# Kernel optimization log

Hardware: AMD Instinct MI355X
Metric: run time of the kernel (lower is better)

## Reference

```python
import jax, jax.numpy as jnp
import numpy as np

B, N, D, H = 2, 2048, 1024, 16
DH = D // H  # 64


def setup_inputs() -> dict:
    key = jax.random.key(0)
    k1, k2, k3, k4, k5 = jax.random.split(key, 5)
    x = jax.random.normal(k1, (B, N, D), dtype=jnp.float32)
    # per-head kqv Linear weights, stacked: [H, D, 3*DH] (acts as x @ W)
    W_kqv = jax.random.normal(k2, (H, D, 3 * DH), dtype=jnp.float32) * 0.02
    b_kqv = jax.random.normal(k3, (H, 3 * DH), dtype=jnp.float32) * 0.02
    W_proj = jax.random.normal(k4, (D, D), dtype=jnp.float32) * 0.02
    b_proj = jax.random.normal(k5, (D,), dtype=jnp.float32) * 0.02
    return {"x": x, "W_kqv": W_kqv, "b_kqv": b_kqv, "W_proj": W_proj, "b_proj": b_proj}


def reference(x, W_kqv, b_kqv, W_proj, b_proj):
    # per-head projections, all heads batched: [B, H, N, 3*DH]
    kqv = jnp.einsum('bnd,hde->bhne', x, W_kqv) + b_kqv[None, :, None, :]
    # original chunk order is k, q, v
    k, q, v = jnp.split(kqv, 3, axis=-1)  # each [B, H, N, DH]
    # scores: A = q @ k^T / sqrt(DH)  -> [B, H, N, N]
    A = jnp.einsum('bhnd,bhmd->bhnm', q, k) / jnp.sqrt(jnp.asarray(DH, x.dtype))
    causal = jnp.tril(jnp.ones((N, N), dtype=bool))
    A = jnp.where(causal[None, None, :, :], A, -jnp.inf)
    attn = jax.nn.softmax(A, axis=-1)
    sa = jnp.einsum('bhnm,bhmd->bhnd', attn, v)          # [B, H, N, DH]
    sa = sa.transpose(0, 2, 1, 3).reshape(B, N, D)        # concat heads
    out = sa @ W_proj.T + b_proj                          # output projection
    return out
```

## Files before the change

kernel.cpp:

```cpp
#include <hip/hip_runtime.h>
#include <hip/hip_bf16.h>
#include <cstdint>
#include <cstddef>

#define B_  2
#define N_  2048
#define D_  1024
#define H_  16
#define DH_ 64
#define E3_ 192

typedef __attribute__((ext_vector_type(8))) short short8;
typedef __attribute__((ext_vector_type(8))) unsigned short ushort8v;
typedef __attribute__((ext_vector_type(4))) float floatx4;

static __device__ __forceinline__ unsigned short f2bf(float f) {
  union { float f; unsigned u; } c; c.f = f;
  unsigned r = c.u + 0x7fffu + ((c.u >> 16) & 1u);
  return (unsigned short)(r >> 16);
}

#define MFMA(a,b,c) __builtin_amdgcn_mfma_f32_16x16x32_bf16((a),(b),(c),0,0,0)

#define GL_LDS16(g, l) __builtin_amdgcn_global_load_lds( \
    (const __attribute__((address_space(1))) void*)(g),  \
    (__attribute__((address_space(3))) void*)(l), 16, 0, 0)

__global__ __launch_bounds__(256) void k_prep(const float* __restrict__ x,
                                              const float* __restrict__ Wkqv,
                                              const float* __restrict__ Wproj,
                                              unsigned short* __restrict__ Xb,
                                              unsigned short* __restrict__ Wt,
                                              unsigned short* __restrict__ Wpb) {
  __shared__ float tile[64][65];
  int bx = blockIdx.x, t = threadIdx.x;
  if (bx < 2048 || bx >= 2816) {
    const float* in = (bx < 2048) ? x : Wproj;
    unsigned short* out = (bx < 2048) ? Xb : Wpb;
    int i = ((bx < 2048) ? bx : bx - 2816) * 256 + t;
    const float4* p = (const float4*)in + (size_t)i * 2;
    float4 a = p[0], b = p[1];
    ushort8v o;
    o[0]=f2bf(a.x); o[1]=f2bf(a.y); o[2]=f2bf(a.z); o[3]=f2bf(a.w);
    o[4]=f2bf(b.x); o[5]=f2bf(b.y); o[6]=f2bf(b.z); o[7]=f2bf(b.w);
    *((ushort8v*)out + i) = o;
    return;
  }
  int idx = bx - 2048;
  int d0 = (idx & 15) * 64, rem = idx >> 4;
  int cat = rem % 3, h = rem / 3, e0 = cat * 64;
  const float* Wp = Wkqv + (size_t)h * D_ * E3_;
  int dr = t >> 2, ec = (t & 3) * 16;
#pragma unroll
  for (int j = 0; j < 16; j += 4) {
    float4 wv = *(const float4*)&Wp[(size_t)(d0 + dr) * E3_ + e0 + ec + j];
    tile[dr][ec + j + 0] = wv.x; tile[dr][ec + j + 1] = wv.y;
    tile[dr][ec + j + 2] = wv.z; tile[dr][ec + j + 3] = wv.w;
  }
  __syncthreads();
  int er = t >> 2, dc = (t & 3) * 16;
  ushort8v o0, o1;
#pragma unroll
  for (int j = 0; j < 8; j++) o0[j] = f2bf(tile[dc + j][er]);
#pragma unroll
  for (int j = 0; j < 8; j++) o1[j] = f2bf(tile[dc + 8 + j][er]);
  size_t o = ((size_t)(cat * 1024 + h * 64 + er)) * D_ + d0 + dc;
  *(ushort8v*)&Wt[o]     = o0;
  *(ushort8v*)&Wt[o + 8] = o1;
}

__global__ __launch_bounds__(512, 2) void k_qkv(const unsigned short* __restrict__ Xb,
                                                const unsigned short* __restrict__ Wt,
                                                const float* __restrict__ bkqv,
                                                unsigned short* __restrict__ Qb,
                                                unsigned short* __restrict__ Kb,
                                                unsigned short* __restrict__ Vt) {
  __shared__ unsigned short LDSf[65536];
  const int t = threadIdx.x;
  const int wid = t >> 6, lane = t & 63, quad = lane >> 4, l16 = lane & 15;
  const int wr = wid >> 2, wc = wid & 3;
  const int m0 = blockIdx.x * 256, c0 = blockIdx.y * 256;

  floatx4 acc[8][4];
#pragma unroll
  for (int i = 0; i < 8; i++)
#pragma unroll
    for (int j = 0; j < 4; j++) acc[i][j] = (floatx4){0.f, 0.f, 0.f, 0.f};

  const int slr = t >> 3;
  const int sco = ((t & 7) ^ (slr & 7)) * 8;
  const unsigned short* gA0 = Xb + (size_t)(m0 +   0 + slr) * D_ + sco;
  const unsigned short* gA1 = Xb + (size_t)(m0 +  64 + slr) * D_ + sco;
  const unsigned short* gA2 = Xb + (size_t)(m0 + 128 + slr) * D_ + sco;
  const unsigned short* gA3 = Xb + (size_t)(m0 + 192 + slr) * D_ + sco;
  const unsigned short* gB0 = Wt + (size_t)(c0 +   0 + slr) * D_ + sco;
  const unsigned short* gB1 = Wt + (size_t)(c0 +  64 + slr) * D_ + sco;
  const unsigned short* gB2 = Wt + (size_t)(c0 + 128 + slr) * D_ + sco;
  const unsigned short* gB3 = Wt + (size_t)(c0 + 192 + slr) * D_ + sco;
#define SA(gp, q, s, bb) GL_LDS16((gp) + (s) * 64, &LDSf[(bb) * 16384 + (q) * 4096 + t * 8])
#define SB(gp, q, s, bb) GL_LDS16((gp) + (s) * 64, &LDSf[32768 + (bb) * 16384 + (q) * 4096 + t * 8])

  const int aoff0 = ((quad)     ^ (l16 & 7)) * 8;
  const int aoff1 = ((4 + quad) ^ (l16 & 7)) * 8;
  const unsigned short* Abase = &LDSf[(wr * 128 + l16) * 64];
  const unsigned short* Bbase = &LDSf[32768 + (wc * 64 + l16) * 64];

  SA(gA0, 0, 0, 0); SA(gA1, 1, 0, 0); SA(gA2, 2, 0, 0); SA(gA3, 3, 0, 0);
  SB(gB0, 0, 0, 0); SB(gB1, 1, 0, 0); SB(gB2, 2, 0, 0); SB(gB3, 3, 0, 0);
  SA(gA0, 0, 1, 1); SA(gA2, 2, 1, 1);
  asm volatile("s_waitcnt vmcnt(2)" ::: "memory");
  __builtin_amdgcn_s_barrier();

  for (int s = 0; s < 16; s++) {
    const int buf = s & 1, nbuf = buf ^ 1;
    const int so = buf * 16384;
    short8 a[4][2], b[4][2];
#pragma unroll
    for (int mi = 0; mi < 4; mi++) {
      a[mi][0] = *(const short8*)&Abase[so + mi * 1024 + aoff0];
      a[mi][1] = *(const short8*)&Abase[so + mi * 1024 + aoff1];
    }
#pragma unroll
    for (int ni = 0; ni < 2; ni++) {
      b[ni][0] = *(const short8*)&Bbase[so + ni * 1024 + aoff0];
      b[ni][1] = *(const short8*)&Bbase[so + ni * 1024 + aoff1];
    }
    if (s < 15) {
      SA(gA1, 1, s + 1, nbuf); SA(gA3, 3, s + 1, nbuf);
      SB(gB0, 0, s + 1, nbuf); SB(gB1, 1, s + 1, nbuf);
      SB(gB2, 2, s + 1, nbuf); SB(gB3, 3, s + 1, nbuf);
    }
    __builtin_amdgcn_s_barrier();
    asm volatile("s_waitcnt lgkmcnt(0)" ::: "memory");
    __builtin_amdgcn_sched_barrier(0);
    __builtin_amdgcn_s_setprio(1);
#pragma unroll
    for (int mi = 0; mi < 4; mi++)
#pragma unroll
      for (int ni = 0; ni < 2; ni++) {
        acc[mi][ni] = MFMA(a[mi][0], b[ni][0], acc[mi][ni]);
        acc[mi][ni] = MFMA(a[mi][1], b[ni][1], acc[mi][ni]);
      }
    __builtin_amdgcn_s_setprio(0);
    __builtin_amdgcn_s_barrier();
#pragma unroll
    for (int ni = 2; ni < 4; ni++) {
      b[ni][0] = *(const short8*)&Bbase[so + ni * 1024 + aoff0];
      b[ni][1] = *(const short8*)&Bbase[so + ni * 1024 + aoff1];
    }
    __builtin_amdgcn_s_barrier();
    asm volatile("s_waitcnt lgkmcnt(0)" ::: "memory");
    __builtin_amdgcn_sched_barrier(0);
    __builtin_amdgcn_s_setprio(1);
#pragma unroll
    for (int mi = 0; mi < 4; mi++)
#pragma unroll
      for (int ni = 2; ni < 4; ni++) {
        acc[mi][ni] = MFMA(a[mi][0], b[ni][0], acc[mi][ni]);
        acc[mi][ni] = MFMA(a[mi][1], b[ni][1], acc[mi][ni]);
      }
    __builtin_amdgcn_s_setprio(0);
    __builtin_amdgcn_s_barrier();
#pragma unroll
    for (int mi = 0; mi < 4; mi++) {
      a[mi][0] = *(const short8*)&Abase[so + (mi + 4) * 1024 + aoff0];
      a[mi][1] = *(const short8*)&Abase[so + (mi + 4) * 1024 + aoff1];
    }
    if (s < 14) { SA(gA0, 0, s + 2, buf); SA(gA2, 2, s + 2, buf); }
    __builtin_amdgcn_s_barrier();
    asm volatile("s_waitcnt lgkmcnt(0)" ::: "memory");
    __builtin_amdgcn_sched_barrier(0);
    __builtin_amdgcn_s_setprio(1);
#pragma unroll
    for (int mi = 0; mi < 4; mi++)
#pragma unroll
      for (int ni = 0; ni < 2; ni++) {
        acc[mi + 4][ni] = MFMA(a[mi][0], b[ni][0], acc[mi + 4][ni]);
        acc[mi + 4][ni] = MFMA(a[mi][1], b[ni][1], acc[mi + 4][ni]);
      }
    __builtin_amdgcn_s_setprio(0);
    __builtin_amdgcn_s_barrier();
    __builtin_amdgcn_s_setprio(1);
#pragma unroll
    for (int mi = 0; mi < 4; mi++)
#pragma unroll
      for (int ni = 2; ni < 4; ni++) {
        acc[mi + 4][ni] = MFMA(a[mi][0], b[ni][0], acc[mi + 4][ni]);
        acc[mi + 4][ni] = MFMA(a[mi][1], b[ni][1], acc[mi + 4][ni]);
      }
    __builtin_amdgcn_s_setprio(0);
    if (s < 14) { asm volatile("s_waitcnt vmcnt(2)" ::: "memory"); }
    else        { asm volatile("s_waitcnt vmcnt(0)" ::: "memory"); }
    __builtin_amdgcn_s_barrier();
  }

  __syncthreads();
  unsigned short* scr = &LDSf[wid * 8192];
  const int cat = c0 >> 10;
  const int h   = ((c0 + wc * 64) >> 6) & 15;
  const int bb  = (m0 + wr * 128) >> 11;
  const int n0b = (m0 + wr * 128) & (N_ - 1);
  const int l8 = lane & 7, lh = lane >> 3;
  if (cat < 2) {
    const float scale = (cat == 1) ? 0.18033688011112042f : 1.0f;
    float bias[4];
#pragma unroll
    for (int ni = 0; ni < 4; ni++) bias[ni] = bkqv[h * E3_ + cat * 64 + ni * 16 + l16];
#pragma unroll
    for (int mi = 0; mi < 8; mi++)
#pragma unroll
      for (int ni = 0; ni < 4; ni++)
#pragma unroll
        for (int r = 0; r < 4; r++) {
          int rl = mi * 16 + quad * 4 + r, cl = ni * 16 + l16;
          scr[rl * 64 + ((((cl >> 3) ^ rl) & 7) * 8) + (cl & 7)] =
              f2bf((acc[mi][ni][r] + bias[ni]) * scale);
        }
    asm volatile("s_waitcnt lgkmcnt(0)" ::: "memory");
    unsigned short* dst = (cat == 0) ? Kb : Qb;
#pragma unroll
    for (int j = 0; j < 16; j++) {
      int rl = j * 8 + lh;
      short8 vv = *(const short8*)&scr[rl * 64 + ((l8 ^ lh) * 8)];
      *(short8*)&dst[((size_t)(bb * H_ + h) * N_ + n0b + rl) * DH_ + l8 * 8] = vv;
    }
  } else {
    float bias[4];
#pragma unroll
    for (int ni = 0; ni < 4; ni++) bias[ni] = bkqv[h * E3_ + 128 + ni * 16 + l16];
#pragma unroll
    for (int mi = 0; mi < 8; mi++)
#pragma unroll
      for (int ni = 0; ni < 4; ni++)
#pragma unroll
        for (int r = 0; r < 4; r++) {
          int nl = mi * 16 + quad * 4 + r, e = ni * 16 + l16;
          scr[e * 128 + ((((nl >> 3) ^ e) & 15) * 8) + (nl & 7)] =
              f2bf(acc[mi][ni][r] + bias[ni]);
        }
    asm volatile("s_waitcnt lgkmcnt(0)" ::: "memory");
#pragma unroll
    for (int j = 0; j < 16; j++) {
      int e = (j & 7) * 8 + lh;
      int nc = l8 + (j >> 3) * 8;
      short8 vv = *(const short8*)&scr[e * 128 + (((nc ^ e) & 15) * 8)];
      *(short8*)&Vt[((size_t)(bb * H_ + h) * DH_ + e) * N_ + n0b + nc * 8] = vv;
    }
  }
#undef SA
#undef SB
}

__global__ __launch_bounds__(256) void k_flash(const unsigned short* __restrict__ Qb,
                                               const unsigned short* __restrict__ Kb,
                                               const unsigned short* __restrict__ Vt,
                                               unsigned short* __restrict__ sab) {
  int bh = blockIdx.x;
  int yr = blockIdx.y, g = yr >> 3, o = yr & 7;
  int qb = (g == 0) ? o : (g == 1) ? 31 - o : (g == 2) ? 8 + o : 23 - o;
  int q0b = qb * 64;
  int wave = threadIdx.x >> 6;
  int lane = threadIdx.x & 63, quad = lane >> 4, l16 = lane & 15;
  const unsigned short* Qp = Qb + (size_t)bh * N_ * DH_;
  const unsigned short* Kp = Kb + (size_t)bh * N_ * DH_;
  const unsigned short* Vp = Vt + (size_t)bh * DH_ * N_;
  __shared__ unsigned short Klds[2][2 * 64 * 32];
  __shared__ unsigned short Vlds[2][2 * 64 * 32];
  __shared__ unsigned short Plds[4][16 * 64];
  unsigned short* P = Plds[wave];

  int q0w = q0b + wave * 16;
  short8 qf0 = *(const short8*)&Qp[(q0w + l16) * DH_ + quad * 8];
  short8 qf1 = *(const short8*)&Qp[(q0w + l16) * DH_ + 32 + quad * 8];

  int swz = ((lane & 3) ^ ((lane >> 3) & 3)) * 8;
  const unsigned short* gK = Kp + (size_t)(wave * 16 + (lane >> 2)) * DH_ + swz;
  const unsigned short* gV = Vp + (size_t)(wave * 16 + (lane >> 2)) * N_ + swz;
  int lofs = (wave * 16) * 32;
  int xr = ((l16 >> 1) & 3) * 8;
  int pxr = l16 & 7;

#define FSTAGE(ii, bb) do {                                              \
    size_t ko_ = (size_t)(ii) * 64 * DH_; int vo_ = (ii) * 64;           \
    GL_LDS16(gK + ko_,      &Klds[bb][lofs]);                            \
    GL_LDS16(gK + ko_ + 32, &Klds[bb][lofs + 64 * 32]);                  \
    GL_LDS16(gV + vo_,      &Vlds[bb][lofs]);                            \
    GL_LDS16(gV + vo_ + 32, &Vlds[bb][lofs + 64 * 32]);                  \
  } while (0)

  floatx4 O[4];
  float lr[4];
#pragma unroll
  for (int r = 0; r < 4; r++) { O[r] = (floatx4){0.f, 0.f, 0.f, 0.f}; lr[r] = 0.f; }

  int nt = (q0b >> 6) + 1;
  FSTAGE(0, 0);
  if (nt > 1) FSTAGE(1, 1);

  for (int i = 0; i < nt; i++) {
    int buf = i & 1;
    if (i + 1 < nt) { asm volatile("s_waitcnt vmcnt(4)" ::: "memory"); }
    else            { asm volatile("s_waitcnt vmcnt(0)" ::: "memory"); }
    __builtin_amdgcn_s_barrier();
    __builtin_amdgcn_sched_barrier(0);
    short8 kf[4][2], vf[4][2];
#pragma unroll
    for (int c = 0; c < 4; c++) {
      kf[c][0] = *(const short8*)&Klds[buf][(c * 16 + l16) * 32 + ((quad * 8) ^ xr)];
      kf[c][1] = *(const short8*)&Klds[buf][(64 + c * 16 + l16) * 32 + ((quad * 8) ^ xr)];
      vf[c][0] = *(const short8*)&Vlds[buf][(c * 16 + l16) * 32 + ((quad * 8) ^ xr)];
      vf[c][1] = *(const short8*)&Vlds[buf][(64 + c * 16 + l16) * 32 + ((quad * 8) ^ xr)];
    }
    floatx4 s[4];
#pragma unroll
    for (int c = 0; c < 4; c++) {
      s[c] = (floatx4){0.f, 0.f, 0.f, 0.f};
      s[c] = MFMA(qf0, kf[c][0], s[c]);
      s[c] = MFMA(qf1, kf[c][1], s[c]);
    }
    if (i == nt - 1) {
#pragma unroll
      for (int c = 0; c < 4; c++)
#pragma unroll
        for (int r = 0; r < 4; r++) {
          int row = wave * 16 + quad * 4 + r;
          if (c * 16 + l16 > row) s[c][r] = -1e30f;
        }
    }
#pragma unroll
    for (int c = 0; c < 4; c++)
#pragma unroll
      for (int r = 0; r < 4; r++)
        s[c][r] = __builtin_amdgcn_exp2f(s[c][r]);
#pragma unroll
    for (int r = 0; r < 4; r++)
      lr[r] += (s[0][r] + s[1][r]) + (s[2][r] + s[3][r]);
#pragma unroll
    for (int c = 0; c < 4; c++) {
      int ch = c * 2 + (l16 >> 3);
#pragma unroll
      for (int r = 0; r < 4; r++) {
        int row = quad * 4 + r;
        P[row * 64 + ((ch ^ (row & 7)) * 8) + (l16 & 7)] = f2bf(s[c][r]);
      }
    }
    __asm__ volatile("s_waitcnt lgkmcnt(0)" ::: "memory");
    short8 pa0 = *(const short8*)&P[l16 * 64 + ((quad ^ pxr) * 8)];
    short8 pa1 = *(const short8*)&P[l16 * 64 + (((quad + 4) ^ pxr) * 8)];
    __asm__ volatile("" ::: "memory");
#pragma unroll
    for (int dt = 0; dt < 4; dt++) {
      O[dt] = MFMA(pa0, vf[dt][0], O[dt]);
      O[dt] = MFMA(pa1, vf[dt][1], O[dt]);
    }
    __builtin_amdgcn_s_barrier();
    __builtin_amdgcn_sched_barrier(0);
    if (i + 2 < nt) FSTAGE(i + 2, buf);
  }
#undef FSTAGE

#pragma unroll
  for (int m = 1; m < 16; m <<= 1)
#pragma unroll
    for (int r = 0; r < 4; r++) lr[r] += __shfl_xor(lr[r], m);

  int b = bh >> 4, h = bh & 15;
#pragma unroll
  for (int r = 0; r < 4; r++) {
    float inv = 1.0f / lr[r];
    size_t base = ((size_t)b * N_ + q0w + quad * 4 + r) * D_ + h * DH_;
#pragma unroll
    for (int dt = 0; dt < 4; dt++) sab[base + dt * 16 + l16] = f2bf(O[dt][r] * inv);
  }
}

__global__ __launch_bounds__(256) void k_proj(const unsigned short* __restrict__ sab,
                                              const unsigned short* __restrict__ Wpb,
                                              const float* __restrict__ bproj,
                                              float* __restrict__ out) {
  __shared__ unsigned short Alds[2][2][64 * 32];
  __shared__ unsigned short Blds[2][2][64 * 32];
  int t = threadIdx.x;
  int m0 = blockIdx.x * 64, c0 = blockIdx.y * 64;
  int wave = t >> 6, lane = t & 63, quad = lane >> 4, l16 = lane & 15;
  int wm = (wave >> 1) * 32, wn = (wave & 1) * 32;
  floatx4 acc[2][2];
#pragma unroll
  for (int i = 0; i < 2; i++) { acc[i][0] = (floatx4){0,0,0,0}; acc[i][1] = (floatx4){0,0,0,0}; }

  int swz = ((lane & 3) ^ ((lane >> 3) & 3)) * 8;
  const unsigned short* gA = sab + (size_t)(m0 + wave * 16 + (lane >> 2)) * D_ + swz;
  const unsigned short* gB = Wpb + (size_t)(c0 + wave * 16 + (lane >> 2)) * D_ + swz;
  int lofs = (wave * 16) * 32;
  int xr = ((l16 >> 1) & 3) * 8;

  GL_LDS16(gA,      &Alds[0][0][lofs]);
  GL_LDS16(gA + 32, &Alds[0][1][lofs]);
  GL_LDS16(gB,      &Blds[0][0][lofs]);
  GL_LDS16(gB + 32, &Blds[0][1][lofs]);

  for (int i = 0; i < 16; i++) {
    int buf = i & 1;
    __syncthreads();
    if (i + 1 < 16) {
      int k0 = (i + 1) * 64;
      GL_LDS16(gA + k0,      &Alds[buf ^ 1][0][lofs]);
      GL_LDS16(gA + k0 + 32, &Alds[buf ^ 1][1][lofs]);
      GL_LDS16(gB + k0,      &Blds[buf ^ 1][0][lofs]);
      GL_LDS16(gB + k0 + 32, &Blds[buf ^ 1][1][lofs]);
    }
#pragma unroll
    for (int kk = 0; kk < 2; kk++) {
      short8 a[2], b[2];
#pragma unroll
      for (int mi = 0; mi < 2; mi++) a[mi] = *(const short8*)&Alds[buf][kk][(wm + mi * 16 + l16) * 32 + ((quad * 8) ^ xr)];
#pragma unroll
      for (int ni = 0; ni < 2; ni++) b[ni] = *(const short8*)&Blds[buf][kk][(wn + ni * 16 + l16) * 32 + ((quad * 8) ^ xr)];
#pragma unroll
      for (int mi = 0; mi < 2; mi++)
#pragma unroll
        for (int ni = 0; ni < 2; ni++) acc[mi][ni] = MFMA(a[mi], b[ni], acc[mi][ni]);
    }
  }
#pragma unroll
  for (int mi = 0; mi < 2; mi++)
#pragma unroll
    for (int ni = 0; ni < 2; ni++) {
      int col = c0 + wn + ni * 16 + l16;
      int grow = m0 + wm + mi * 16 + quad * 4;
      float bias = bproj[col];
#pragma unroll
      for (int r = 0; r < 4; r++)
        out[(size_t)(grow + r) * D_ + col] = acc[mi][ni][r] + bias;
    }
}

extern "C" void kernel_launch(void* const* d_in, const int* in_sizes, int n_in,
                              void* d_out, int out_size, void* d_ws, size_t ws_size,
                              hipStream_t stream) {
  const float* x     = (const float*)d_in[0];
  const float* Wkqv  = (const float*)d_in[1];
  const float* bkqv  = (const float*)d_in[2];
  const float* Wproj = (const float*)d_in[3];
  const float* bproj = (const float*)d_in[4];
  float* out = (float*)d_out;

  char* w = (char*)d_ws;
  unsigned short* Xb  = (unsigned short*)(w);
  unsigned short* Wt  = (unsigned short*)(w + (8u  << 20));
  unsigned short* Wpb = (unsigned short*)(w + (14u << 20));
  unsigned short* Qb  = (unsigned short*)(w + (16u << 20));
  unsigned short* Kb  = (unsigned short*)(w + (24u << 20));
  unsigned short* Vt  = (unsigned short*)(w + (32u << 20));
  unsigned short* sa  = (unsigned short*)(w + (40u << 20));

  k_prep<<<2048 + 768 + 512, 256, 0, stream>>>(x, Wkqv, Wproj, Xb, Wt, Wpb);
  k_qkv<<<dim3(B_ * N_ / 256, 3072 / 256), 512, 0, stream>>>(Xb, Wt, bkqv, Qb, Kb, Vt);
  k_flash<<<dim3(B_ * H_, N_ / 64), 256, 0, stream>>>(Qb, Kb, Vt, sa);
  k_proj<<<dim3(B_ * N_ / 64, D_ / 64), 256, 0, stream>>>(sa, Wpb, bproj, out);
}
```

Before: 172.5 us.

## Retile output projection GEMM to 128x128 blocks with deeper prefetch; add MFMA setprio

The output projection kernel moves from 64x64 tiles with 4 waves to 128x128 tiles with 8 waves. It uses a single swizzled LDS buffer with a two-stage-ahead global_load_lds prefetch and explicit vmcnt waits, which raises operand reuse per load and reduces global traffic. The flash-attention and projection MFMA sections are also wrapped in s_setprio raises so waves doing matrix math are favored. The trade-offs are fewer blocks (256 instead of 1024), which may leave CUs underused, and higher register and LDS pressure per block.

```diff
diff --git a/kernel.cpp b/kernel.cpp
--- a/kernel.cpp
+++ b/kernel.cpp
@@ -312,12 +312,14 @@
       vf[c][1] = *(const short8*)&Vlds[buf][(64 + c * 16 + l16) * 32 + ((quad * 8) ^ xr)];
     }
     floatx4 s[4];
+    __builtin_amdgcn_s_setprio(1);
 #pragma unroll
     for (int c = 0; c < 4; c++) {
       s[c] = (floatx4){0.f, 0.f, 0.f, 0.f};
       s[c] = MFMA(qf0, kf[c][0], s[c]);
       s[c] = MFMA(qf1, kf[c][1], s[c]);
     }
+    __builtin_amdgcn_s_setprio(0);
     if (i == nt - 1) {
 #pragma unroll
       for (int c = 0; c < 4; c++)
@@ -348,11 +350,13 @@
     short8 pa0 = *(const short8*)&P[l16 * 64 + ((quad ^ pxr) * 8)];
     short8 pa1 = *(const short8*)&P[l16 * 64 + (((quad + 4) ^ pxr) * 8)];
     __asm__ volatile("" ::: "memory");
+    __builtin_amdgcn_s_setprio(1);
 #pragma unroll
     for (int dt = 0; dt < 4; dt++) {
       O[dt] = MFMA(pa0, vf[dt][0], O[dt]);
       O[dt] = MFMA(pa1, vf[dt][1], O[dt]);
     }
+    __builtin_amdgcn_s_setprio(0);
     __builtin_amdgcn_s_barrier();
     __builtin_amdgcn_sched_barrier(0);
     if (i + 2 < nt) FSTAGE(i + 2, buf);
@@ -374,65 +378,88 @@
   }
 }
 
-__global__ __launch_bounds__(256) void k_proj(const unsigned short* __restrict__ sab,
+__global__ __launch_bounds__(512) void k_proj(const unsigned short* __restrict__ sab,
                                               const unsigned short* __restrict__ Wpb,
                                               const float* __restrict__ bproj,
                                               float* __restrict__ out) {
-  __shared__ unsigned short Alds[2][2][64 * 32];
-  __shared__ unsigned short Blds[2][2][64 * 32];
-  int t = threadIdx.x;
-  int m0 = blockIdx.x * 64, c0 = blockIdx.y * 64;
-  int wave = t >> 6, lane = t & 63, quad = lane >> 4, l16 = lane & 15;
-  int wm = (wave >> 1) * 32, wn = (wave & 1) * 32;
-  floatx4 acc[2][2];
-#pragma unroll
-  for (int i = 0; i < 2; i++) { acc[i][0] = (floatx4){0,0,0,0}; acc[i][1] = (floatx4){0,0,0,0}; }
-
-  int swz = ((lane & 3) ^ ((lane >> 3) & 3)) * 8;
-  const unsigned short* gA = sab + (size_t)(m0 + wave * 16 + (lane >> 2)) * D_ + swz;
-  const unsigned short* gB = Wpb + (size_t)(c0 + wave * 16 + (lane >> 2)) * D_ + swz;
-  int lofs = (wave * 16) * 32;
-  int xr = ((l16 >> 1) & 3) * 8;
-
-  GL_LDS16(gA,      &Alds[0][0][lofs]);
-  GL_LDS16(gA + 32, &Alds[0][1][lofs]);
-  GL_LDS16(gB,      &Blds[0][0][lofs]);
-  GL_LDS16(gB + 32, &Blds[0][1][lofs]);
+  __shared__ unsigned short LDSp[32768];
+  const int t = threadIdx.x;
+  const int wid = t >> 6, lane = t & 63, quad = lane >> 4, l16 = lane & 15;
+  const int wr = wid >> 1, wc = wid & 1;
+  const int bid = blockIdx.x;
+  const int m0 = (bid >> 3) * 128, c0 = (bid & 7) * 128;
+
+  floatx4 acc[2][4];
+#pragma unroll
+  for (int i = 0; i < 2; i++)
+#pragma unroll
+    for (int j = 0; j < 4; j++) acc[i][j] = (floatx4){0.f, 0.f, 0.f, 0.f};
+
+  const int slr = t >> 3;
+  const int sco = ((t & 7) ^ (slr & 7)) * 8;
+  const unsigned short* gA0 = sab + (size_t)(m0 +  0 + slr) * D_ + sco;
+  const unsigned short* gA1 = sab + (size_t)(m0 + 64 + slr) * D_ + sco;
+  const unsigned short* gB0 = Wpb + (size_t)(c0 +  0 + slr) * D_ + sco;
+  const unsigned short* gB1 = Wpb + (size_t)(c0 + 64 + slr) * D_ + sco;
+#define PA(gp, q, s, bb) GL_LDS16((gp) + (s) * 64, &LDSp[(bb) * 8192 + (q) * 4096 + t * 8])
+#define PB(gp, q, s, bb) GL_LDS16((gp) + (s) * 64, &LDSp[16384 + (bb) * 8192 + (q) * 4096 + t * 8])
+
+  const int aoff0 = ((quad)     ^ (l16 & 7)) * 8;
+  const int aoff1 = ((4 + quad) ^ (l16 & 7)) * 8;
+  const unsigned short* Abase = &LDSp[(wr * 32 + l16) * 64];
+  const unsigned short* Bbase = &LDSp[16384 + (wc * 64 + l16) * 64];
+
+  PA(gA0, 0, 0, 0); PA(gA1, 1, 0, 0); PB(gB0, 0, 0, 0); PB(gB1, 1, 0, 0);
+  PA(gA0, 0, 1, 1); PA(gA1, 1, 1, 1); PB(gB0, 0, 1, 1); PB(gB1, 1, 1, 1);
 
   for (int i = 0; i < 16; i++) {
-    int buf = i & 1;
-    __syncthreads();
-    if (i + 1 < 16) {
-      int k0 = (i + 1) * 64;
-      GL_LDS16(gA + k0,      &Alds[buf ^ 1][0][lofs]);
-      GL_LDS16(gA + k0 + 32, &Alds[buf ^ 1][1][lofs]);
-      GL_LDS16(gB + k0,      &Blds[buf ^ 1][0][lofs]);
-      GL_LDS16(gB + k0 + 32, &Blds[buf ^ 1][1][lofs]);
-    }
-#pragma unroll
-    for (int kk = 0; kk < 2; kk++) {
-      short8 a[2], b[2];
-#pragma unroll
-      for (int mi = 0; mi < 2; mi++) a[mi] = *(const short8*)&Alds[buf][kk][(wm + mi * 16 + l16) * 32 + ((quad * 8) ^ xr)];
-#pragma unroll
-      for (int ni = 0; ni < 2; ni++) b[ni] = *(const short8*)&Blds[buf][kk][(wn + ni * 16 + l16) * 32 + ((quad * 8) ^ xr)];
-#pragma unroll
-      for (int mi = 0; mi < 2; mi++)
-#pragma unroll
-        for (int ni = 0; ni < 2; ni++) acc[mi][ni] = MFMA(a[mi], b[ni], acc[mi][ni]);
-    }
-  }
+    const int buf = i & 1;
+    const int so = buf * 8192;
+    if (i + 1 < 16) { asm volatile("s_waitcnt vmcnt(4)" ::: "memory"); }
+    else            { asm volatile("s_waitcnt vmcnt(0)" ::: "memory"); }
+    __builtin_amdgcn_s_barrier();
+    __builtin_amdgcn_sched_barrier(0);
+    short8 a[2][2], b[4][2];
+#pragma unroll
+    for (int mi = 0; mi < 2; mi++) {
+      a[mi][0] = *(const short8*)&Abase[so + mi * 1024 + aoff0];
+      a[mi][1] = *(const short8*)&Abase[so + mi * 1024 + aoff1];
+    }
+#pragma unroll
+    for (int ni = 0; ni < 4; ni++) {
+      b[ni][0] = *(const short8*)&Bbase[so + ni * 1024 + aoff0];
+      b[ni][1] = *(const short8*)&Bbase[so + ni * 1024 + aoff1];
+    }
+    __builtin_amdgcn_s_setprio(1);
+#pragma unroll
+    for (int mi = 0; mi < 2; mi++)
+#pragma unroll
+      for (int ni = 0; ni < 4; ni++) {
+        acc[mi][ni] = MFMA(a[mi][0], b[ni][0], acc[mi][ni]);
+        acc[mi][ni] = MFMA(a[mi][1], b[ni][1], acc[mi][ni]);
+      }
+    __builtin_amdgcn_s_setprio(0);
+    __builtin_amdgcn_s_barrier();
+    __builtin_amdgcn_sched_barrier(0);
+    if (i + 2 < 16) {
+      PA(gA0, 0, i + 2, buf); PA(gA1, 1, i + 2, buf);
+      PB(gB0, 0, i + 2, buf); PB(gB1, 1, i + 2, buf);
+    }
+  }
+
 #pragma unroll
   for (int mi = 0; mi < 2; mi++)
 #pragma unroll
-    for (int ni = 0; ni < 2; ni++) {
-      int col = c0 + wn + ni * 16 + l16;
-      int grow = m0 + wm + mi * 16 + quad * 4;
+    for (int ni = 0; ni < 4; ni++) {
+      int col = c0 + wc * 64 + ni * 16 + l16;
+      int grow = m0 + wr * 32 + mi * 16 + quad * 4;
       float bias = bproj[col];
 #pragma unroll
       for (int r = 0; r < 4; r++)
         out[(size_t)(grow + r) * D_ + col] = acc[mi][ni][r] + bias;
     }
+#undef PA
+#undef PB
 }
 
 extern "C" void kernel_launch(void* const* d_in, const int* in_sizes, int n_in,
@@ -457,5 +484,5 @@
   k_prep<<<2048 + 768 + 512, 256, 0, stream>>>(x, Wkqv, Wproj, Xb, Wt, Wpb);
   k_qkv<<<dim3(B_ * N_ / 256, 3072 / 256), 512, 0, stream>>>(Xb, Wt, bkqv, Qb, Kb, Vt);
   k_flash<<<dim3(B_ * H_, N_ / 64), 256, 0, stream>>>(Qb, Kb, Vt, sa);
-  k_proj<<<dim3(B_ * N_ / 64, D_ / 64), 256, 0, stream>>>(sa, Wpb, bproj, out);
-}
+  k_proj<<<(B_ * N_ / 128) * (D_ / 128), 512, 0, stream>>>(sa, Wpb, bproj, out);
+}
```

New measurement: 170.8 us. Within noise of the previous version (-1.0%).
